# Kernel optimization log

Hardware: AMD Instinct MI355X
Metric: run time of the kernel (lower is better)

The kernel has to match this reference:

```python
import jax, jax.numpy as jnp
import numpy as np
from jax import lax

NC = 80
REG_MAX = 16
BINS = REG_MAX + 1
RADIUS = 2.5
TOPK = 10
L_BOX, L_CLS, L_DFL = 7.5, 1.0, 1.5


def focal_bce(x, t, alpha=0.25, gamma=2.0):
    # numerically stable BCE-with-logits: max(x,0) - x*t + log1p(exp(-|x|))
    p = jax.nn.sigmoid(x)
    ce = jnp.maximum(x, 0.0) - x * t + jnp.log1p(jnp.exp(-jnp.abs(x)))
    p_t = p * t + (1.0 - p) * (1.0 - t)
    a_t = alpha * t + (1.0 - alpha) * (1.0 - t)
    return ce * a_t * (1.0 - p_t) ** gamma


def _level_loss(reg, cls, boxes, labels, stride):
    B, _, H, W = reg.shape
    HW = H * W
    G = boxes.shape[1]
    gy, gx = jnp.meshgrid(jnp.arange(H, dtype=jnp.float32), jnp.arange(W, dtype=jnp.float32), indexing='ij')
    centers = jnp.stack([gx + 0.5, gy + 0.5], -1).reshape(HW, 2)  # [HW,2]
    gt = boxes / stride  # [B,G,4]
    gctr = (gt[..., :2] + gt[..., 2:]) * 0.5  # [B,G,2]
    cx = centers[None, :, None, 0]
    cy = centers[None, :, None, 1]
    dl = cx - gt[:, None, :, 0]
    dt = cy - gt[:, None, :, 1]
    dr = gt[:, None, :, 2] - cx
    db = gt[:, None, :, 3] - cy
    in_gt = (dl > 0) & (dt > 0) & (dr > 0) & (db > 0)
    in_ctr = ((cx >= gctr[:, None, :, 0] - RADIUS) & (cx <= gctr[:, None, :, 0] + RADIUS)
              & (cy >= gctr[:, None, :, 1] - RADIUS) & (cy <= gctr[:, None, :, 1] + RADIUS))
    mask = in_gt & in_ctr  # [B,HW,G]
    any_pos = jnp.any(mask, axis=(1, 2))  # [B]
    # fallback: topk closest anchor centers per GT (smallest distance along point dim)
    dist = jnp.sqrt(((centers[None, :, None, :] - gctr[:, None, :, :]) ** 2).sum(-1))  # [B,HW,G]
    k = min(TOPK, HW)
    _, idx = lax.top_k(-jnp.swapaxes(dist, 1, 2), k)  # [B,G,k]
    fb = jnp.zeros((B, HW, G), bool).at[jnp.arange(B)[:, None, None], idx, jnp.arange(G)[None, :, None]].set(True)
    mask = jnp.where(any_pos[:, None, None], mask, fb)
    mf = mask.astype(jnp.float32)
    n_pos = mf.sum((1, 2))  # [B] (>=1 by construction of fallback)

    cls_flat = cls.transpose(0, 2, 3, 1).reshape(B, HW, NC)
    reg_flat = reg.transpose(0, 2, 3, 1).reshape(B, HW, 4, BINS)

    # ---- DFL ----
    ltrb = jnp.clip(jnp.stack([dl, dt, dr, db], -1), 0.0)  # [B,HW,G,4]
    tgt = jnp.clip(ltrb, 0.0, REG_MAX - 1e-4)
    lb = jnp.floor(tgt).astype(jnp.int32)
    rb = jnp.minimum(lb + 1, REG_MAX)
    wl = rb.astype(jnp.float32) - tgt
    wr = tgt - lb.astype(jnp.float32)
    logp = jax.nn.log_softmax(reg_flat, -1)  # [B,HW,4,BINS]
    bi = jnp.arange(B)[:, None, None, None]
    pi = jnp.arange(HW)[None, :, None, None]
    ki = jnp.arange(4)[None, None, None, :]
    dfl_pair = -(logp[bi, pi, ki, lb] * wl + logp[bi, pi, ki, rb] * wr)  # [B,HW,G,4]
    dfl = ((dfl_pair * mf[..., None]).sum((1, 2, 3)) / (n_pos * 4.0)).sum()

    # ---- box (IoU, detached as in original) ----
    prob = jax.nn.softmax(reg_flat, -1)
    d = (prob * jnp.arange(BINS, dtype=jnp.float32)).sum(-1)  # [B,HW,4]
    pcx = centers[None, :, 0]
    pcy = centers[None, :, 1]
    pred_box = jnp.stack([pcx - d[..., 0], pcy - d[..., 1], pcx + d[..., 2], pcy + d[..., 3]], -1)  # [B,HW,4]
    b1 = pred_box[:, :, None, :]
    b2 = gt[:, None, :, :]
    iw = jnp.clip(jnp.minimum(b1[..., 2:], b2[..., 2:]) - jnp.maximum(b1[..., :2], b2[..., :2]), 0.0)
    inter = iw[..., 0] * iw[..., 1]
    a1 = (b1[..., 2] - b1[..., 0]) * (b1[..., 3] - b1[..., 1])
    a2 = (b2[..., 2] - b2[..., 0]) * (b2[..., 3] - b2[..., 1])
    iou = lax.stop_gradient(inter / (a1 + a2 - inter + 1e-6))  # [B,HW,G]
    box = ((1.0 - iou) * mf).sum()

    # ---- cls (focal BCE, soft IoU targets). Decompose one-hot target:
    # per positive pair: sum_c f(logit_c,0) - f(logit_cls,0) + f(logit_cls,iou)
    fz = focal_bce(cls_flat, 0.0)  # [B,HW,NC]
    fz_sum = fz.sum(-1)  # [B,HW]
    bi2 = jnp.arange(B)[:, None, None]
    pi2 = jnp.arange(HW)[None, :, None]
    ci = labels[:, None, :]  # [B,1,G]
    cls_at = cls_flat[bi2, pi2, ci]  # [B,HW,G]
    fz_at = fz[bi2, pi2, ci]
    cls_pos = ((fz_sum[:, :, None] - fz_at + focal_bce(cls_at, iou)) * mf).sum()
    pos_pt = jnp.any(mask, -1)  # [B,HW]
    cls_neg = jnp.where(pos_pt, 0.0, fz_sum).sum()
    return box, cls_pos + cls_neg, dfl


def _total(reg0, cls0, reg1, cls1, reg2, cls2, gt_boxes, gt_labels):
    tb = tc = td = 0.0
    for r, c, s in ((reg0, cls0, 8.0), (reg1, cls1, 16.0), (reg2, cls2, 32.0)):
        b, cl, d = _level_loss(r, c, gt_boxes, gt_labels, s)
        tb = tb + b
        tc = tc + cl
        td = td + d
    loss = L_BOX * tb + L_CLS * tc + L_DFL * td
    return loss, tb, tc, td


def setup_inputs() -> dict:
    key = jax.random.key(0)
    ks = jax.random.split(key, 10)
    B, G = 16, 32
    d = {}
    for i, (h, w) in enumerate(((80, 80), (40, 40), (20, 20))):
        d[f'reg{i}'] = jax.random.normal(ks[2 * i], (B, 4 * BINS, h, w), jnp.float32)
        d[f'cls{i}'] = jax.random.normal(ks[2 * i + 1], (B, NC, h, w), jnp.float32)
    ctr = jax.random.uniform(ks[6], (B, G, 2), minval=0.0, maxval=640.0)
    wh = jax.random.uniform(ks[7], (B, G, 2), minval=16.0, maxval=160.0)
    x1y1 = jnp.clip(ctr - wh * 0.5, 0.0, 640.0)
    x2y2 = jnp.clip(ctr + wh * 0.5, 0.0, 640.0)
    d['gt_boxes'] = jnp.concatenate([x1y1, x2y2], -1)
    d['gt_labels'] = jax.random.randint(ks[8], (B, G), 0, NC, jnp.int32)
    return d


def reference(reg0, cls0, reg1, cls1, reg2, cls2, gt_boxes, gt_labels):
    return _total(reg0, cls0, reg1, cls1, reg2, cls2, gt_boxes, gt_labels)
```

## Files before the change

kernel.cpp:

```cpp
#include <hip/hip_runtime.h>
#include <math.h>

#define NCLS 80
#define BINS 17
#define REGMAX 16
#define NG 32
#define NB 16
#define KTOP 10
#define RAD 2.5f

#define WS_ACC   0
#define WS_NPOS  32
#define WS_DFLN  224
#define WS_CNT   608
#define NBLOCKS  (34 * 16)

__device__ __forceinline__ float focal0(float x) {
    float e   = __expf(-fabsf(x));
    float inv = 1.0f / (1.0f + e);
    float p   = (x >= 0.0f) ? inv : e * inv;
    float ce  = fmaxf(x, 0.0f) + __logf(1.0f + e);
    return ce * 0.75f * p * p;
}

__device__ __forceinline__ float focal_t(float x, float t) {
    float e   = __expf(-fabsf(x));
    float inv = 1.0f / (1.0f + e);
    float p   = (x >= 0.0f) ? inv : e * inv;
    float ce  = fmaxf(x, 0.0f) - x * t + __logf(1.0f + e);
    float pt  = p * t + (1.0f - p) * (1.0f - t);
    float at  = 0.25f * t + 0.75f * (1.0f - t);
    float om  = 1.0f - pt;
    return ce * at * om * om;
}

__global__ __launch_bounds__(512, 2) void k_main_f(
    const float* __restrict__ reg0, const float* __restrict__ cls0,
    const float* __restrict__ reg1, const float* __restrict__ cls1,
    const float* __restrict__ reg2, const float* __restrict__ cls2,
    const float* __restrict__ gtb,  const int* __restrict__ lab,
    float* __restrict__ acc, float* __restrict__ npos, float* __restrict__ dfln,
    int* __restrict__ cnt, float* __restrict__ out)
{
    int bx = blockIdx.x;
    int b  = blockIdx.y;
    int lvl, tix, W; const float *regp, *clsp; float inv_s;
    if (bx < 25)      { lvl = 0; tix = bx;      W = 80; regp = reg0; clsp = cls0; inv_s = 0.125f;   }
    else if (bx < 32) { lvl = 1; tix = bx - 25; W = 40; regp = reg1; clsp = cls1; inv_s = 0.0625f;  }
    else              { lvl = 2; tix = bx - 32; W = 20; regp = reg2; clsp = cls2; inv_s = 0.03125f; }
    int HW = W * W;
    int tile = tix * 256;

    int tid  = threadIdx.x;
    int lane = tid & 63;
    int w    = tid >> 6;
    int p0   = tile + 4 * lane;
    bool v   = p0 < HW;
    int pb   = v ? p0 : HW - 4;

    __shared__ float s_bx[NG][6];
    __shared__ int   s_lab[NG];
    __shared__ float s_dv[4][256], s_lz[4][256], s_fzp[4][256], s_fzs[256];
    __shared__ unsigned char s_ps[8][64];
    __shared__ float red[8][4];
    __shared__ int   s_any, s_tick, s_fb[NG][KTOP];

    if (tid == 0) s_any = 0;
    if (tid < NG) {
        int g = tid;
        float4 bb4 = *(const float4*)(gtb + (b * NG + g) * 4);
        float x1 = bb4.x * inv_s, y1 = bb4.y * inv_s;
        float x2 = bb4.z * inv_s, y2 = bb4.w * inv_s;
        s_bx[g][0] = x1; s_bx[g][1] = y1; s_bx[g][2] = x2; s_bx[g][3] = y2;
        s_bx[g][4] = (x1 + x2) * 0.5f; s_bx[g][5] = (y1 + y2) * 0.5f;
        s_lab[g] = lab[b * NG + g];
    }
    __syncthreads();

    {
        int g = tid >> 4, wi = tid & 15;
        float x1 = s_bx[g][0], y1 = s_bx[g][1];
        float x2 = s_bx[g][2], y2 = s_bx[g][3];
        float gcx = s_bx[g][4], gcy = s_bx[g][5];
        int jc = (int)floorf(gcx), ic = (int)floorf(gcy);
        bool any = false;
#pragma unroll
        for (int r = 0; r < 6; ++r) {
            int ci = wi + 16 * r;
            if (ci < 81) {
                int j = jc + (ci % 9) - 4, i = ic + (ci / 9) - 4;
                if (j >= 0 && j < W && i >= 0 && i < W) {
                    float cx = (float)j + 0.5f, cy = (float)i + 0.5f;
                    bool m = (cx - x1 > 0.0f) && (cy - y1 > 0.0f) &&
                             (x2 - cx > 0.0f) && (y2 - cy > 0.0f) &&
                             (cx >= gcx - RAD) && (cx <= gcx + RAD) &&
                             (cy >= gcy - RAD) && (cy <= gcy + RAD);
                    any = any || m;
                }
            }
        }
        if (__any(any) && lane == 0) atomicOr(&s_any, 1);
    }
    __syncthreads();
    bool anyb = s_any != 0;

    if (!anyb) {
        if (tid < NG) {
            int g = tid;
            float gcx = s_bx[g][4], gcy = s_bx[g][5];
            float bd[KTOP]; int bi[KTOP];
            for (int t = 0; t < KTOP; ++t) { bd[t] = 3.0e38f; bi[t] = 0; }
            for (int p = 0; p < HW; ++p) {
                float cx = (float)(p % W) + 0.5f;
                float cy = (float)(p / W) + 0.5f;
                float dx = cx - gcx, dy = cy - gcy;
                float d = dx * dx + dy * dy;
                if (d < bd[KTOP - 1]) {
                    int t = KTOP - 1;
                    while (t > 0 && d < bd[t - 1]) { bd[t] = bd[t-1]; bi[t] = bi[t-1]; --t; }
                    bd[t] = d; bi[t] = p;
                }
            }
            for (int t = 0; t < KTOP; ++t) s_fb[g][t] = bi[t];
        }
        __syncthreads();
    }

    if (w < 4) {
        const float* bp = regp + (size_t)(b * 68 + w * BINS) * HW + pb;
        float4 rv[BINS];
#pragma unroll
        for (int t = 0; t < BINS; ++t)
            rv[t] = *(const float4*)(bp + (size_t)t * HW);
        asm volatile("s_waitcnt vmcnt(0)" ::: "memory");
        __builtin_amdgcn_sched_barrier(0);
        float m[4], sm[4], ex[4];
#pragma unroll
        for (int j = 0; j < 4; ++j) { m[j] = -3.0e38f; sm[j] = 0.f; ex[j] = 0.f; }
#pragma unroll
        for (int t = 0; t < BINS; ++t) {
            float xv[4] = { rv[t].x, rv[t].y, rv[t].z, rv[t].w };
#pragma unroll
            for (int j = 0; j < 4; ++j) m[j] = fmaxf(m[j], xv[j]);
        }
#pragma unroll
        for (int t = 0; t < BINS; ++t) {
            float xv[4] = { rv[t].x, rv[t].y, rv[t].z, rv[t].w };
#pragma unroll
            for (int j = 0; j < 4; ++j) {
                float e = __expf(xv[j] - m[j]);
                sm[j] += e; ex[j] += e * (float)t;
            }
        }
        *(float4*)&s_dv[w][4 * lane] =
            make_float4(ex[0] / sm[0], ex[1] / sm[1], ex[2] / sm[2], ex[3] / sm[3]);
        *(float4*)&s_lz[w][4 * lane] =
            make_float4(__logf(sm[0]) + m[0], __logf(sm[1]) + m[1],
                        __logf(sm[2]) + m[2], __logf(sm[3]) + m[3]);
    } else {
        int q = w - 4;
        const float* bp = clsp + (size_t)(b * 80 + q * 20) * HW + pb;
        float4 cv[20];
#pragma unroll
        for (int t = 0; t < 20; ++t)
            cv[t] = *(const float4*)(bp + (size_t)t * HW);
        asm volatile("s_waitcnt vmcnt(0)" ::: "memory");
        __builtin_amdgcn_sched_barrier(0);
        float fz[4] = { 0.f, 0.f, 0.f, 0.f };
#pragma unroll
        for (int t = 0; t < 20; ++t) {
            fz[0] += focal0(cv[t].x); fz[1] += focal0(cv[t].y);
            fz[2] += focal0(cv[t].z); fz[3] += focal0(cv[t].w);
        }
        *(float4*)&s_fzp[q][4 * lane] = make_float4(fz[0], fz[1], fz[2], fz[3]);
    }
    __syncthreads();

    if (tid < 256)
        s_fzs[tid] = s_fzp[0][tid] + s_fzp[1][tid] + s_fzp[2][tid] + s_fzp[3][tid];
    __syncthreads();

    float bxa = 0.f, cla = 0.f, dfa = 0.f, np = 0.f;
    unsigned posm = 0;
    int ri = p0 / W;
    float cy  = (float)ri + 0.5f;
    float cxb = (float)(p0 - ri * W) + 0.5f;

    if (v) {
        int r0 = tile / W, r1 = min(tile + 255, HW - 1) / W;
        float cyLo = (float)r0 + 0.5f, cyHi = (float)r1 + 0.5f;
#pragma unroll
        for (int gi = 0; gi < 4; ++gi) {
            int g = w + 8 * gi;
            float x1 = s_bx[g][0], y1 = s_bx[g][1];
            float x2 = s_bx[g][2], y2 = s_bx[g][3];
            float gx = s_bx[g][4], gy = s_bx[g][5];
            if (anyb) {
                if (!((cyHi > y1) && (y2 > cyLo) &&
                      (cyHi >= gy - RAD) && (cyLo <= gy + RAD))) continue;
            }
#pragma unroll
            for (int j = 0; j < 4; ++j) {
                float cx = cxb + (float)j;
                float dl = cx - x1, dt = cy - y1, dr = x2 - cx, db = y2 - cy;
                bool mk;
                if (anyb) {
                    mk = (dl > 0.f) && (dt > 0.f) && (dr > 0.f) && (db > 0.f) &&
                         (cx >= gx - RAD) && (cx <= gx + RAD) &&
                         (cy >= gy - RAD) && (cy <= gy + RAD);
                } else {
                    int pt = p0 + j;
                    mk = false;
                    for (int t = 0; t < KTOP; ++t) mk = mk || (s_fb[g][t] == pt);
                }
                if (mk) {
                    posm |= (1u << j);
                    np += 1.f;
                    int ptl = 4 * lane + j, pt = p0 + j;
                    float dv0 = s_dv[0][ptl], dv1 = s_dv[1][ptl];
                    float dv2 = s_dv[2][ptl], dv3 = s_dv[3][ptl];
                    float px1 = cx - dv0, py1 = cy - dv1;
                    float px2 = cx + dv2, py2 = cy + dv3;
                    float pa = (px2 - px1) * (py2 - py1);
                    float ix1 = fmaxf(px1, x1), iy1 = fmaxf(py1, y1);
                    float ix2 = fminf(px2, x2), iy2 = fminf(py2, y2);
                    float iw = fmaxf(ix2 - ix1, 0.f), ih = fmaxf(iy2 - iy1, 0.f);
                    float inter = iw * ih;
                    float ga = (x2 - x1) * (y2 - y1);
                    float iou = inter / (pa + ga - inter + 1e-6f);
                    bxa += 1.f - iou;
                    float ltrb[4] = { dl, dt, dr, db };
#pragma unroll
                    for (int k = 0; k < 4; ++k) {
                        float tt = fminf(fmaxf(ltrb[k], 0.f), 15.9999f);
                        float lf = floorf(tt); int lb = (int)lf;
                        int rb = lb + 1 > REGMAX ? REGMAX : lb + 1;
                        float wl = (float)rb - tt, wr = tt - lf;
                        float lzk = s_lz[k][ptl];
                        float xl = regp[(size_t)(b * 68 + k * BINS + lb) * HW + pt];
                        float xr = regp[(size_t)(b * 68 + k * BINS + rb) * HW + pt];
                        dfa -= (xl - lzk) * wl + (xr - lzk) * wr;
                    }
                    int cc = s_lab[g];
                    float xat = clsp[(size_t)(b * 80 + cc) * HW + pt];
                    cla += s_fzs[ptl] - focal0(xat) + focal_t(xat, iou);
                }
            }
        }
    }
    s_ps[w][lane] = (unsigned char)posm;
    __syncthreads();

    if (tid < 256 && tile + tid < HW) {
        unsigned pg = 0;
#pragma unroll
        for (int wv = 0; wv < 8; ++wv) pg |= s_ps[wv][tid >> 2];
        if (!((pg >> (tid & 3)) & 1u)) cla += s_fzs[tid];
    }

    float v0 = bxa, v1 = cla, v2 = dfa, v3 = np;
    for (int off = 32; off > 0; off >>= 1) {
        v0 += __shfl_down(v0, off);
        v1 += __shfl_down(v1, off);
        v2 += __shfl_down(v2, off);
        v3 += __shfl_down(v3, off);
    }
    if (lane == 0) { red[w][0] = v0; red[w][1] = v1; red[w][2] = v2; red[w][3] = v3; }
    __syncthreads();
    if (tid == 0) {
        float t0 = 0, t1 = 0, t2 = 0, t3 = 0;
        for (int wv = 0; wv < 8; ++wv) {
            t0 += red[wv][0]; t1 += red[wv][1]; t2 += red[wv][2]; t3 += red[wv][3];
        }
        atomicAdd(&acc[0], t0);
        atomicAdd(&acc[1], t1);
        atomicAdd(&dfln[lvl * NB + b], t2);
        atomicAdd(&npos[lvl * NB + b], t3);
    }

    if (tid == 0) {
        __threadfence();
        s_tick = atomicAdd(cnt, 1);
    }
    __syncthreads();
    if (s_tick == NBLOCKS - 1 && tid < 64) {
        float vs = 0.f;
        if (lane < 48) {
            float n = atomicAdd(&npos[lane], 0.0f);
            float d = atomicAdd(&dfln[lane], 0.0f);
            if (n > 0.f) vs = d / (n * 4.0f);
        }
        for (int off = 32; off > 0; off >>= 1) vs += __shfl_down(vs, off);
        if (lane == 0) {
            float tbv = atomicAdd(&acc[0], 0.0f);
            float tcv = atomicAdd(&acc[1], 0.0f);
            out[0] = 7.5f * tbv + tcv + 1.5f * vs;
            out[1] = tbv; out[2] = tcv; out[3] = vs;
        }
    }
}

extern "C" void kernel_launch(void* const* d_in, const int* in_sizes, int n_in,
                              void* d_out, int out_size, void* d_ws, size_t ws_size,
                              hipStream_t stream) {
    const float* reg0 = (const float*)d_in[0];
    const float* cls0 = (const float*)d_in[1];
    const float* reg1 = (const float*)d_in[2];
    const float* cls1 = (const float*)d_in[3];
    const float* reg2 = (const float*)d_in[4];
    const float* cls2 = (const float*)d_in[5];
    const float* gtb  = (const float*)d_in[6];
    const int*   lab  = (const int*)d_in[7];
    float* out = (float*)d_out;

    char*  ws   = (char*)d_ws;
    float* acc  = (float*)(ws + WS_ACC);
    float* npos = (float*)(ws + WS_NPOS);
    float* dfln = (float*)(ws + WS_DFLN);
    int*   cnt  = (int*)(ws + WS_CNT);

    hipMemsetAsync(d_ws, 0, 612, stream);
    k_main_f<<<dim3(34, NB), 512, 0, stream>>>(reg0, cls0, reg1, cls1, reg2, cls2,
                                               gtb, lab,
                                               acc, npos, dfln, cnt, out);
}
```

Before: 58.69 us.

## Split loss into streaming softmax/focal pass and per-anchor assignment pass

Adds a first kernel that streams all reg and cls planes with many blocks, computing per-anchor DFL expectation, log-sum-exp and background focal sums into a large workspace. A second, lighter kernel then does GT assignment per anchor and reads those precomputed values. The aim is to spread the bandwidth-heavy work over more blocks and cut register pressure in the assignment pass. The cost is an extra launch plus workspace round trips. The streaming softmax drops max-subtraction, so large logits could overflow. The fallback kernel also switches to online softmax with interleaved loads.

```diff
diff --git a/kernel.cpp b/kernel.cpp
--- a/kernel.cpp
+++ b/kernel.cpp
@@ -9,11 +9,14 @@
 #define KTOP 10
 #define RAD 2.5f
 
-#define WS_ACC   0
-#define WS_NPOS  32
-#define WS_DFLN  224
-#define WS_CNT   608
-#define NBLOCKS  (34 * 16)
+#define PLANE    134400
+#define FZP_OFF  256
+#define DV_OFF   (256 + 8 * PLANE)
+#define LZ_OFF   (256 + 12 * PLANE)
+#define WS_NEED  ((size_t)(256 + 16 * PLANE) * 4)
+#define NBLOCKS_B (34 * 16)
+
+__device__ __constant__ int c_lvlbase[3] = { 0, 102400, 128000 };
 
 __device__ __forceinline__ float focal0(float x) {
     float e   = __expf(-fabsf(x));
@@ -34,7 +37,295 @@
     return ce * at * om * om;
 }
 
-__global__ __launch_bounds__(512, 2) void k_main_f(
+__global__ __launch_bounds__(512) void k_stream(
+    const float* __restrict__ reg0, const float* __restrict__ cls0,
+    const float* __restrict__ reg1, const float* __restrict__ cls1,
+    const float* __restrict__ reg2, const float* __restrict__ cls2,
+    float* __restrict__ ws)
+{
+    int id  = blockIdx.x;
+    int tid = threadIdx.x;
+    if (id < 192) {
+        int lvl = id / 64, rem = id % 64, b = rem / 4, k = rem % 4;
+        const float* regp = (lvl == 0) ? reg0 : (lvl == 1 ? reg1 : reg2);
+        int W  = (lvl == 0) ? 80 : (lvl == 1 ? 40 : 20);
+        int HW = W * W;
+        const float* base = regp + (size_t)(b * 68 + k * BINS) * HW;
+        float sm[16], ex[16];
+#pragma unroll
+        for (int i = 0; i < 16; ++i) { sm[i] = 0.f; ex[i] = 0.f; }
+        for (int t = 0; t < BINS; ++t) {
+            const float* rb = base + (size_t)t * HW;
+            float tf = (float)t;
+#pragma unroll
+            for (int j = 0; j < 4; ++j) {
+                int p = tid * 4 + 2048 * j;
+                if (p < HW) {
+                    float4 x = *(const float4*)(rb + p);
+                    float e0 = __expf(x.x), e1 = __expf(x.y);
+                    float e2 = __expf(x.z), e3 = __expf(x.w);
+                    sm[j*4+0] += e0; ex[j*4+0] += e0 * tf;
+                    sm[j*4+1] += e1; ex[j*4+1] += e1 * tf;
+                    sm[j*4+2] += e2; ex[j*4+2] += e2 * tf;
+                    sm[j*4+3] += e3; ex[j*4+3] += e3 * tf;
+                }
+            }
+        }
+        int pidx = c_lvlbase[lvl] + b * HW;
+#pragma unroll
+        for (int j = 0; j < 4; ++j) {
+            int p = tid * 4 + 2048 * j;
+            if (p < HW) {
+                float4 dv4 = make_float4(ex[j*4+0] / sm[j*4+0], ex[j*4+1] / sm[j*4+1],
+                                         ex[j*4+2] / sm[j*4+2], ex[j*4+3] / sm[j*4+3]);
+                float4 lz4 = make_float4(__logf(sm[j*4+0]), __logf(sm[j*4+1]),
+                                         __logf(sm[j*4+2]), __logf(sm[j*4+3]));
+                *(float4*)(ws + DV_OFF + (size_t)k * PLANE + pidx + p) = dv4;
+                *(float4*)(ws + LZ_OFF + (size_t)k * PLANE + pidx + p) = lz4;
+            }
+        }
+    } else {
+        int id2 = id - 192;
+        int lvl = id2 / 128, rem = id2 % 128, b = rem / 8, cg = rem % 8;
+        const float* clsp = (lvl == 0) ? cls0 : (lvl == 1 ? cls1 : cls2);
+        int W  = (lvl == 0) ? 80 : (lvl == 1 ? 40 : 20);
+        int HW = W * W;
+        const float* base = clsp + (size_t)(b * 80 + cg * 10) * HW;
+        float fz[16];
+#pragma unroll
+        for (int i = 0; i < 16; ++i) fz[i] = 0.f;
+        for (int t = 0; t < 10; ++t) {
+            const float* rb = base + (size_t)t * HW;
+#pragma unroll
+            for (int j = 0; j < 4; ++j) {
+                int p = tid * 4 + 2048 * j;
+                if (p < HW) {
+                    float4 x = *(const float4*)(rb + p);
+                    fz[j*4+0] += focal0(x.x); fz[j*4+1] += focal0(x.y);
+                    fz[j*4+2] += focal0(x.z); fz[j*4+3] += focal0(x.w);
+                }
+            }
+        }
+        int pidx = c_lvlbase[lvl] + b * HW;
+#pragma unroll
+        for (int j = 0; j < 4; ++j) {
+            int p = tid * 4 + 2048 * j;
+            if (p < HW) {
+                *(float4*)(ws + FZP_OFF + (size_t)cg * PLANE + pidx + p) =
+                    make_float4(fz[j*4+0], fz[j*4+1], fz[j*4+2], fz[j*4+3]);
+            }
+        }
+    }
+}
+
+__global__ __launch_bounds__(256) void k_finish(
+    const float* __restrict__ reg0, const float* __restrict__ cls0,
+    const float* __restrict__ reg1, const float* __restrict__ cls1,
+    const float* __restrict__ reg2, const float* __restrict__ cls2,
+    const float* __restrict__ gtb,  const int* __restrict__ lab,
+    float* __restrict__ ws, float* __restrict__ out)
+{
+    float* acc  = ws;
+    float* npos = ws + 8;
+    float* dfln = ws + 56;
+    int*   cnt  = (int*)(ws + 152);
+
+    int bx = blockIdx.x;
+    int b  = blockIdx.y;
+    int lvl, tix, W; const float *regp, *clsp; float inv_s;
+    if (bx < 25)      { lvl = 0; tix = bx;      W = 80; regp = reg0; clsp = cls0; inv_s = 0.125f;   }
+    else if (bx < 32) { lvl = 1; tix = bx - 25; W = 40; regp = reg1; clsp = cls1; inv_s = 0.0625f;  }
+    else              { lvl = 2; tix = bx - 32; W = 20; regp = reg2; clsp = cls2; inv_s = 0.03125f; }
+    int HW = W * W;
+    int tile = tix * 256;
+
+    int tid  = threadIdx.x;
+    int lane = tid & 63;
+    int w    = tid >> 6;
+    int pt   = tile + tid;
+    bool v   = pt < HW;
+    int pidx = c_lvlbase[lvl] + b * HW + (v ? pt : 0);
+
+    __shared__ float s_bx[NG][6];
+    __shared__ int   s_lab[NG];
+    __shared__ int   s_any, s_tick, s_fb[NG][KTOP];
+    __shared__ float red[4][4];
+
+    if (tid == 0) s_any = 0;
+    if (tid < NG) {
+        int g = tid;
+        float4 bb4 = *(const float4*)(gtb + (b * NG + g) * 4);
+        float x1 = bb4.x * inv_s, y1 = bb4.y * inv_s;
+        float x2 = bb4.z * inv_s, y2 = bb4.w * inv_s;
+        s_bx[g][0] = x1; s_bx[g][1] = y1; s_bx[g][2] = x2; s_bx[g][3] = y2;
+        s_bx[g][4] = (x1 + x2) * 0.5f; s_bx[g][5] = (y1 + y2) * 0.5f;
+        s_lab[g] = lab[b * NG + g];
+    }
+    __syncthreads();
+
+    {
+        int g = tid >> 3, wi = tid & 7;
+        float x1 = s_bx[g][0], y1 = s_bx[g][1];
+        float x2 = s_bx[g][2], y2 = s_bx[g][3];
+        float gcx = s_bx[g][4], gcy = s_bx[g][5];
+        int jc = (int)floorf(gcx), ic = (int)floorf(gcy);
+        bool any = false;
+#pragma unroll
+        for (int r = 0; r < 11; ++r) {
+            int ci = wi + 8 * r;
+            if (ci < 81) {
+                int j = jc + (ci % 9) - 4, i = ic + (ci / 9) - 4;
+                if (j >= 0 && j < W && i >= 0 && i < W) {
+                    float cx = (float)j + 0.5f, cy = (float)i + 0.5f;
+                    bool m = (cx - x1 > 0.0f) && (cy - y1 > 0.0f) &&
+                             (x2 - cx > 0.0f) && (y2 - cy > 0.0f) &&
+                             (cx >= gcx - RAD) && (cx <= gcx + RAD) &&
+                             (cy >= gcy - RAD) && (cy <= gcy + RAD);
+                    any = any || m;
+                }
+            }
+        }
+        if (__any(any) && lane == 0) atomicOr(&s_any, 1);
+    }
+    __syncthreads();
+    bool anyb = s_any != 0;
+
+    if (!anyb) {
+        if (tid < NG) {
+            int g = tid;
+            float gcx = s_bx[g][4], gcy = s_bx[g][5];
+            float bd[KTOP]; int bi[KTOP];
+            for (int t = 0; t < KTOP; ++t) { bd[t] = 3.0e38f; bi[t] = 0; }
+            for (int p = 0; p < HW; ++p) {
+                float cx = (float)(p % W) + 0.5f;
+                float cy = (float)(p / W) + 0.5f;
+                float dx = cx - gcx, dy = cy - gcy;
+                float d = dx * dx + dy * dy;
+                if (d < bd[KTOP - 1]) {
+                    int t = KTOP - 1;
+                    while (t > 0 && d < bd[t - 1]) { bd[t] = bd[t-1]; bi[t] = bi[t-1]; --t; }
+                    bd[t] = d; bi[t] = p;
+                }
+            }
+            for (int t = 0; t < KTOP; ++t) s_fb[g][t] = bi[t];
+        }
+        __syncthreads();
+    }
+
+    float fz = 0.f;
+    if (v) {
+#pragma unroll
+        for (int cg = 0; cg < 8; ++cg)
+            fz += ws[FZP_OFF + (size_t)cg * PLANE + pidx];
+    }
+
+    float bxa = 0.f, cla = 0.f, dfa = 0.f, np = 0.f;
+    bool pos = false, ld = false;
+    float dv0 = 0, dv1 = 0, dv2 = 0, dv3 = 0, lzv[4] = {0, 0, 0, 0};
+    int ri = v ? pt / W : 0;
+    float cy = (float)ri + 0.5f;
+    float cx = (float)(pt - ri * W) + 0.5f;
+
+    if (v) {
+        for (int g = 0; g < NG; ++g) {
+            float x1 = s_bx[g][0], y1 = s_bx[g][1];
+            float x2 = s_bx[g][2], y2 = s_bx[g][3];
+            float dl = cx - x1, dt = cy - y1, dr = x2 - cx, db = y2 - cy;
+            bool mk;
+            if (anyb) {
+                float gx = s_bx[g][4], gy = s_bx[g][5];
+                mk = (dl > 0.f) && (dt > 0.f) && (dr > 0.f) && (db > 0.f) &&
+                     (cx >= gx - RAD) && (cx <= gx + RAD) &&
+                     (cy >= gy - RAD) && (cy <= gy + RAD);
+            } else {
+                mk = false;
+                for (int t = 0; t < KTOP; ++t) mk = mk || (s_fb[g][t] == pt);
+            }
+            if (mk) {
+                pos = true;
+                np += 1.f;
+                if (!ld) {
+                    dv0 = ws[DV_OFF + 0 * PLANE + pidx];
+                    dv1 = ws[DV_OFF + 1 * PLANE + pidx];
+                    dv2 = ws[DV_OFF + 2 * PLANE + pidx];
+                    dv3 = ws[DV_OFF + 3 * PLANE + pidx];
+#pragma unroll
+                    for (int k = 0; k < 4; ++k)
+                        lzv[k] = ws[LZ_OFF + (size_t)k * PLANE + pidx];
+                    ld = true;
+                }
+                float px1 = cx - dv0, py1 = cy - dv1;
+                float px2 = cx + dv2, py2 = cy + dv3;
+                float pa = (px2 - px1) * (py2 - py1);
+                float ix1 = fmaxf(px1, x1), iy1 = fmaxf(py1, y1);
+                float ix2 = fminf(px2, x2), iy2 = fminf(py2, y2);
+                float iw = fmaxf(ix2 - ix1, 0.f), ih = fmaxf(iy2 - iy1, 0.f);
+                float inter = iw * ih;
+                float ga = (x2 - x1) * (y2 - y1);
+                float iou = inter / (pa + ga - inter + 1e-6f);
+                bxa += 1.f - iou;
+                float ltrb[4] = { dl, dt, dr, db };
+#pragma unroll
+                for (int k = 0; k < 4; ++k) {
+                    float tt = fminf(fmaxf(ltrb[k], 0.f), 15.9999f);
+                    float lf = floorf(tt); int lb = (int)lf;
+                    int rb = lb + 1 > REGMAX ? REGMAX : lb + 1;
+                    float wl = (float)rb - tt, wr = tt - lf;
+                    float xl = regp[(size_t)(b * 68 + k * BINS + lb) * HW + pt];
+                    float xr = regp[(size_t)(b * 68 + k * BINS + rb) * HW + pt];
+                    dfa -= (xl - lzv[k]) * wl + (xr - lzv[k]) * wr;
+                }
+                int cc = s_lab[g];
+                float xat = clsp[(size_t)(b * 80 + cc) * HW + pt];
+                cla += fz - focal0(xat) + focal_t(xat, iou);
+            }
+        }
+        if (!pos) cla += fz;
+    }
+
+    float v0 = bxa, v1 = cla, v2 = dfa, v3 = np;
+    for (int off = 32; off > 0; off >>= 1) {
+        v0 += __shfl_down(v0, off);
+        v1 += __shfl_down(v1, off);
+        v2 += __shfl_down(v2, off);
+        v3 += __shfl_down(v3, off);
+    }
+    if (lane == 0) { red[w][0] = v0; red[w][1] = v1; red[w][2] = v2; red[w][3] = v3; }
+    __syncthreads();
+    if (tid == 0) {
+        float t0 = 0, t1 = 0, t2 = 0, t3 = 0;
+        for (int wv = 0; wv < 4; ++wv) {
+            t0 += red[wv][0]; t1 += red[wv][1]; t2 += red[wv][2]; t3 += red[wv][3];
+        }
+        atomicAdd(&acc[0], t0);
+        atomicAdd(&acc[1], t1);
+        atomicAdd(&dfln[lvl * NB + b], t2);
+        atomicAdd(&npos[lvl * NB + b], t3);
+    }
+
+    if (tid == 0) {
+        __threadfence();
+        s_tick = atomicAdd(cnt, 1);
+    }
+    __syncthreads();
+    if (s_tick == NBLOCKS_B - 1 && tid < 64) {
+        float vs = 0.f;
+        if (lane < 48) {
+            float n = atomicAdd(&npos[lane], 0.0f);
+            float d = atomicAdd(&dfln[lane], 0.0f);
+            if (n > 0.f) vs = d / (n * 4.0f);
+        }
+        for (int off = 32; off > 0; off >>= 1) vs += __shfl_down(vs, off);
+        if (lane == 0) {
+            float tbv = atomicAdd(&acc[0], 0.0f);
+            float tcv = atomicAdd(&acc[1], 0.0f);
+            out[0] = 7.5f * tbv + tcv + 1.5f * vs;
+            out[1] = tbv; out[2] = tcv; out[3] = vs;
+        }
+    }
+}
+
+__global__ __launch_bounds__(512, 2) void k_main_fb(
     const float* __restrict__ reg0, const float* __restrict__ cls0,
     const float* __restrict__ reg1, const float* __restrict__ cls1,
     const float* __restrict__ reg2, const float* __restrict__ cls2,
@@ -50,7 +341,6 @@
     else              { lvl = 2; tix = bx - 32; W = 20; regp = reg2; clsp = cls2; inv_s = 0.03125f; }
     int HW = W * W;
     int tile = tix * 256;
-
     int tid  = threadIdx.x;
     int lane = tid & 63;
     int w    = tid >> 6;
@@ -76,7 +366,6 @@
         s_lab[g] = lab[b * NG + g];
     }
     __syncthreads();
-
     {
         int g = tid >> 4, wi = tid & 15;
         float x1 = s_bx[g][0], y1 = s_bx[g][1];
@@ -103,7 +392,6 @@
     }
     __syncthreads();
     bool anyb = s_any != 0;
-
     if (!anyb) {
         if (tid < NG) {
             int g = tid;
@@ -125,31 +413,23 @@
         }
         __syncthreads();
     }
-
     if (w < 4) {
         const float* bp = regp + (size_t)(b * 68 + w * BINS) * HW + pb;
-        float4 rv[BINS];
-#pragma unroll
-        for (int t = 0; t < BINS; ++t)
-            rv[t] = *(const float4*)(bp + (size_t)t * HW);
-        asm volatile("s_waitcnt vmcnt(0)" ::: "memory");
-        __builtin_amdgcn_sched_barrier(0);
         float m[4], sm[4], ex[4];
 #pragma unroll
         for (int j = 0; j < 4; ++j) { m[j] = -3.0e38f; sm[j] = 0.f; ex[j] = 0.f; }
 #pragma unroll
         for (int t = 0; t < BINS; ++t) {
-            float xv[4] = { rv[t].x, rv[t].y, rv[t].z, rv[t].w };
-#pragma unroll
-            for (int j = 0; j < 4; ++j) m[j] = fmaxf(m[j], xv[j]);
-        }
-#pragma unroll
-        for (int t = 0; t < BINS; ++t) {
-            float xv[4] = { rv[t].x, rv[t].y, rv[t].z, rv[t].w };
+            float4 x4 = *(const float4*)(bp + (size_t)t * HW);
+            float xv[4] = { x4.x, x4.y, x4.z, x4.w };
 #pragma unroll
             for (int j = 0; j < 4; ++j) {
-                float e = __expf(xv[j] - m[j]);
-                sm[j] += e; ex[j] += e * (float)t;
+                float nm = fmaxf(m[j], xv[j]);
+                float a  = __expf(m[j] - nm);
+                float bb = __expf(xv[j] - nm);
+                sm[j] = sm[j] * a + bb;
+                ex[j] = ex[j] * a + bb * (float)t;
+                m[j]  = nm;
             }
         }
         *(float4*)&s_dv[w][4 * lane] =
@@ -160,22 +440,16 @@
     } else {
         int q = w - 4;
         const float* bp = clsp + (size_t)(b * 80 + q * 20) * HW + pb;
-        float4 cv[20];
-#pragma unroll
-        for (int t = 0; t < 20; ++t)
-            cv[t] = *(const float4*)(bp + (size_t)t * HW);
-        asm volatile("s_waitcnt vmcnt(0)" ::: "memory");
-        __builtin_amdgcn_sched_barrier(0);
         float fz[4] = { 0.f, 0.f, 0.f, 0.f };
 #pragma unroll
         for (int t = 0; t < 20; ++t) {
-            fz[0] += focal0(cv[t].x); fz[1] += focal0(cv[t].y);
-            fz[2] += focal0(cv[t].z); fz[3] += focal0(cv[t].w);
+            float4 c4 = *(const float4*)(bp + (size_t)t * HW);
+            fz[0] += focal0(c4.x); fz[1] += focal0(c4.y);
+            fz[2] += focal0(c4.z); fz[3] += focal0(c4.w);
         }
         *(float4*)&s_fzp[q][4 * lane] = make_float4(fz[0], fz[1], fz[2], fz[3]);
     }
     __syncthreads();
-
     if (tid < 256)
         s_fzs[tid] = s_fzp[0][tid] + s_fzp[1][tid] + s_fzp[2][tid] + s_fzp[3][tid];
     __syncthreads();
@@ -185,7 +459,6 @@
     int ri = p0 / W;
     float cy  = (float)ri + 0.5f;
     float cxb = (float)(p0 - ri * W) + 0.5f;
-
     if (v) {
         int r0 = tile / W, r1 = min(tile + 255, HW - 1) / W;
         float cyLo = (float)r0 + 0.5f, cyHi = (float)r1 + 0.5f;
@@ -250,14 +523,12 @@
     }
     s_ps[w][lane] = (unsigned char)posm;
     __syncthreads();
-
     if (tid < 256 && tile + tid < HW) {
         unsigned pg = 0;
 #pragma unroll
         for (int wv = 0; wv < 8; ++wv) pg |= s_ps[wv][tid >> 2];
         if (!((pg >> (tid & 3)) & 1u)) cla += s_fzs[tid];
     }
-
     float v0 = bxa, v1 = cla, v2 = dfa, v3 = np;
     for (int off = 32; off > 0; off >>= 1) {
         v0 += __shfl_down(v0, off);
@@ -277,13 +548,12 @@
         atomicAdd(&dfln[lvl * NB + b], t2);
         atomicAdd(&npos[lvl * NB + b], t3);
     }
-
     if (tid == 0) {
         __threadfence();
         s_tick = atomicAdd(cnt, 1);
     }
     __syncthreads();
-    if (s_tick == NBLOCKS - 1 && tid < 64) {
+    if (s_tick == NBLOCKS_B - 1 && tid < 64) {
         float vs = 0.f;
         if (lane < 48) {
             float n = atomicAdd(&npos[lane], 0.0f);
@@ -312,15 +582,17 @@
     const float* gtb  = (const float*)d_in[6];
     const int*   lab  = (const int*)d_in[7];
     float* out = (float*)d_out;
-
-    char*  ws   = (char*)d_ws;
-    float* acc  = (float*)(ws + WS_ACC);
-    float* npos = (float*)(ws + WS_NPOS);
-    float* dfln = (float*)(ws + WS_DFLN);
-    int*   cnt  = (int*)(ws + WS_CNT);
+    float* ws  = (float*)d_ws;
 
     hipMemsetAsync(d_ws, 0, 612, stream);
-    k_main_f<<<dim3(34, NB), 512, 0, stream>>>(reg0, cls0, reg1, cls1, reg2, cls2,
-                                               gtb, lab,
-                                               acc, npos, dfln, cnt, out);
+    if (ws_size >= WS_NEED) {
+        k_stream<<<576, 512, 0, stream>>>(reg0, cls0, reg1, cls1, reg2, cls2, ws);
+        k_finish<<<dim3(34, NB), 256, 0, stream>>>(reg0, cls0, reg1, cls1, reg2, cls2,
+                                                   gtb, lab, ws, out);
+    } else {
+        k_main_fb<<<dim3(34, NB), 512, 0, stream>>>(reg0, cls0, reg1, cls1, reg2, cls2,
+                                                    gtb, lab,
+                                                    ws, ws + 8, ws + 56,
+                                                    (int*)(ws + 152), out);
+    }
 }
```

New measurement: 71.74 us. 1.22x slower.

## Stream loads with online softmax, nontemporal hints, and higher occupancy bound

Applied to the files above, without the earlier changes.

The loss kernel no longer loads all 17 or 20 float4 channels into registers behind an explicit wait. Loads are now interleaved with compute, and the DFL softmax switches to an online (running-max) form. Loads use nontemporal hints, and launch bounds rise from 2 to 4 blocks per CU to cut register pressure and raise occupancy. The cost is extra exps in the online softmax and reliance on the compiler to keep enough loads in flight. The grid is only 544 blocks, so the higher occupancy bound may add little beyond the lower register use.

```diff
diff --git a/kernel.cpp b/kernel.cpp
--- a/kernel.cpp
+++ b/kernel.cpp
@@ -14,6 +14,8 @@
 #define WS_DFLN  224
 #define WS_CNT   608
 #define NBLOCKS  (34 * 16)
+
+typedef float vf4 __attribute__((ext_vector_type(4)));
 
 __device__ __forceinline__ float focal0(float x) {
     float e   = __expf(-fabsf(x));
@@ -34,7 +36,11 @@
     return ce * at * om * om;
 }
 
-__global__ __launch_bounds__(512, 2) void k_main_f(
+__device__ __forceinline__ vf4 ldnt4(const float* p) {
+    return __builtin_nontemporal_load((const vf4*)p);
+}
+
+__global__ __launch_bounds__(512, 4) void k_main_f(
     const float* __restrict__ reg0, const float* __restrict__ cls0,
     const float* __restrict__ reg1, const float* __restrict__ cls1,
     const float* __restrict__ reg2, const float* __restrict__ cls2,
@@ -128,28 +134,21 @@
 
     if (w < 4) {
         const float* bp = regp + (size_t)(b * 68 + w * BINS) * HW + pb;
-        float4 rv[BINS];
-#pragma unroll
-        for (int t = 0; t < BINS; ++t)
-            rv[t] = *(const float4*)(bp + (size_t)t * HW);
-        asm volatile("s_waitcnt vmcnt(0)" ::: "memory");
-        __builtin_amdgcn_sched_barrier(0);
         float m[4], sm[4], ex[4];
 #pragma unroll
         for (int j = 0; j < 4; ++j) { m[j] = -3.0e38f; sm[j] = 0.f; ex[j] = 0.f; }
 #pragma unroll
         for (int t = 0; t < BINS; ++t) {
-            float xv[4] = { rv[t].x, rv[t].y, rv[t].z, rv[t].w };
-#pragma unroll
-            for (int j = 0; j < 4; ++j) m[j] = fmaxf(m[j], xv[j]);
-        }
-#pragma unroll
-        for (int t = 0; t < BINS; ++t) {
-            float xv[4] = { rv[t].x, rv[t].y, rv[t].z, rv[t].w };
+            vf4 x4 = ldnt4(bp + (size_t)t * HW);
+            float xv[4] = { x4.x, x4.y, x4.z, x4.w };
 #pragma unroll
             for (int j = 0; j < 4; ++j) {
-                float e = __expf(xv[j] - m[j]);
-                sm[j] += e; ex[j] += e * (float)t;
+                float nm = fmaxf(m[j], xv[j]);
+                float a  = __expf(m[j] - nm);
+                float bb = __expf(xv[j] - nm);
+                sm[j] = sm[j] * a + bb;
+                ex[j] = ex[j] * a + bb * (float)t;
+                m[j]  = nm;
             }
         }
         *(float4*)&s_dv[w][4 * lane] =
@@ -160,17 +159,12 @@
     } else {
         int q = w - 4;
         const float* bp = clsp + (size_t)(b * 80 + q * 20) * HW + pb;
-        float4 cv[20];
-#pragma unroll
-        for (int t = 0; t < 20; ++t)
-            cv[t] = *(const float4*)(bp + (size_t)t * HW);
-        asm volatile("s_waitcnt vmcnt(0)" ::: "memory");
-        __builtin_amdgcn_sched_barrier(0);
         float fz[4] = { 0.f, 0.f, 0.f, 0.f };
 #pragma unroll
         for (int t = 0; t < 20; ++t) {
-            fz[0] += focal0(cv[t].x); fz[1] += focal0(cv[t].y);
-            fz[2] += focal0(cv[t].z); fz[3] += focal0(cv[t].w);
+            vf4 c4 = ldnt4(bp + (size_t)t * HW);
+            fz[0] += focal0(c4.x); fz[1] += focal0(c4.y);
+            fz[2] += focal0(c4.z); fz[3] += focal0(c4.w);
         }
         *(float4*)&s_fzp[q][4 * lane] = make_float4(fz[0], fz[1], fz[2], fz[3]);
     }
@@ -319,7 +313,7 @@
     float* dfln = (float*)(ws + WS_DFLN);
     int*   cnt  = (int*)(ws + WS_CNT);
 
-    hipMemsetAsync(d_ws, 0, 612, stream);
+    (void)hipMemsetAsync(d_ws, 0, 612, stream);
     k_main_f<<<dim3(34, NB), 512, 0, stream>>>(reg0, cls0, reg1, cls1, reg2, cls2,
                                                gtb, lab,
                                                acc, npos, dfln, cnt, out);
```

Result: slower. 63.13 us (+7.6%).
